# Optimization experiments

Measured on AMD Instinct MI355X. Metric: run time of the kernel, lower is better.

The kernel has to match this reference:

```python
import jax, jax.numpy as jnp
import numpy as np

N, E, IN_DIM, EMBED_DIM, HID_DIM = 10000, 320000, 128, 128, 64
NEG_SLOPE = 0.2


def setup_inputs() -> dict:
    key = jax.random.key(0)
    ks = jax.random.split(key, 7)
    x = jax.random.normal(ks[0], (N, IN_DIM), dtype=jnp.float32)
    edge_index = jax.random.randint(ks[1], (2, E), 0, N, dtype=jnp.int64)
    dense_w = jax.random.normal(ks[2], (IN_DIM, EMBED_DIM), dtype=jnp.float32) / np.sqrt(IN_DIM)
    dense_b = jnp.zeros((EMBED_DIM,), dtype=jnp.float32)
    gat_w = jax.random.normal(ks[3], (EMBED_DIM, HID_DIM), dtype=jnp.float32) / np.sqrt(EMBED_DIM)
    att_src = jax.random.normal(ks[4], (HID_DIM,), dtype=jnp.float32) * 0.1
    att_dst = jax.random.normal(ks[5], (HID_DIM,), dtype=jnp.float32) * 0.1
    gat_b = jnp.zeros((HID_DIM,), dtype=jnp.float32)
    return {"x": x, "edge_index": edge_index, "dense_w": dense_w, "dense_b": dense_b,
            "gat_w": gat_w, "att_src": att_src, "att_dst": att_dst, "gat_b": gat_b}


def reference(x, edge_index, dense_w, dense_b, gat_w, att_src, att_dst, gat_b):
    n = x.shape[0]
    # dense + relu
    h = jax.nn.relu(x @ dense_w + dense_b)            # [N, embed]
    # GATConv (heads=1): linear transform
    z = h @ gat_w                                     # [N, hid]
    # add self loops (PyG default)
    loops = jnp.arange(n, dtype=edge_index.dtype)
    src = jnp.concatenate([edge_index[0], loops])     # [E+N] message source j
    dst = jnp.concatenate([edge_index[1], loops])     # [E+N] message target i
    a_src = z @ att_src                               # [N]
    a_dst = z @ att_dst                               # [N]
    e = jax.nn.leaky_relu(a_src[src] + a_dst[dst], NEG_SLOPE)  # [E+N]
    # segment softmax over incoming edges of each target node
    m = jax.ops.segment_max(e, dst, num_segments=n)
    ex = jnp.exp(e - m[dst])
    denom = jax.ops.segment_sum(ex, dst, num_segments=n)
    alpha = ex / denom[dst]                           # [E+N]
    embed_x = jax.ops.segment_sum(alpha[:, None] * z[src], dst, num_segments=n) + gat_b  # [N, hid]
    # pairwise sigmoid similarity
    sim = jax.nn.sigmoid(embed_x @ embed_x.T)         # [N, N]
    return sim, embed_x
```

## Files before the change

### kernel.cpp

```cpp
#include <hip/hip_runtime.h>
#include <math.h>

#define N_NODES 10000
#define E_EDGES 320000
#define IN_DIM 128
#define EMB 128
#define HID 64
#define NEG_SLOPE 0.2f

typedef __attribute__((ext_vector_type(8))) short short8;
typedef __attribute__((ext_vector_type(4))) short short4_t;
typedef __attribute__((ext_vector_type(4))) float floatx4;
typedef __attribute__((ext_vector_type(4))) int   intx4;
typedef __attribute__((ext_vector_type(2))) int   intx2;

__device__ __forceinline__ short f2bf(float f) {
    unsigned u = __float_as_uint(f);
    unsigned r = u + 0x7fffu + ((u >> 16) & 1u);
    return (short)(r >> 16);
}

__device__ __forceinline__ float sigmoidf_fast(float v) {
    return __builtin_amdgcn_rcpf(1.f + __expf(-v));
}

__global__ __launch_bounds__(256) void dense_gat_kernel(
    const float* __restrict__ x, const float* __restrict__ dw,
    const float* __restrict__ db, const float* __restrict__ gw,
    const float* __restrict__ asv, const float* __restrict__ adv,
    float* __restrict__ z, float* __restrict__ a_src, float* __restrict__ a_dst)
{
    __shared__ float xs[16][IN_DIM];
    __shared__ float hs[16][EMB];
    __shared__ float wsm[32 * 128];
    const int t = threadIdx.x;
    const int row0 = blockIdx.x * 16;

    #pragma unroll
    for (int r = 0; r < 2; ++r) {
        const int idx = t + r * 256;
        const int row = idx >> 5, c4 = idx & 31;
        *(floatx4*)&xs[row][c4 * 4] =
            *(const floatx4*)&x[(row0 + row) * IN_DIM + c4 * 4];
    }

    const int col = t & 127, rb = (t >> 7) * 8;
    float acc[8];
    {
        const float bias = db[col];
        #pragma unroll
        for (int r = 0; r < 8; ++r) acc[r] = bias;
    }
    for (int ch = 0; ch < 4; ++ch) {
        __syncthreads();
        #pragma unroll
        for (int r = 0; r < 4; ++r) {
            const int idx = t + r * 256;
            const int row = idx >> 5, c4 = idx & 31;
            *(floatx4*)&wsm[row * 128 + c4 * 4] =
                *(const floatx4*)&dw[(ch * 32 + row) * EMB + c4 * 4];
        }
        __syncthreads();
        #pragma unroll
        for (int jg = 0; jg < 8; ++jg) {
            const int jb = jg * 4;
            floatx4 xr[8];
            #pragma unroll
            for (int r = 0; r < 8; ++r)
                xr[r] = *(const floatx4*)&xs[rb + r][ch * 32 + jb];
            float wv[4];
            #pragma unroll
            for (int k = 0; k < 4; ++k) wv[k] = wsm[(jb + k) * 128 + col];
            #pragma unroll
            for (int k = 0; k < 4; ++k)
                #pragma unroll
                for (int r = 0; r < 8; ++r) acc[r] = fmaf(xr[r][k], wv[k], acc[r]);
        }
    }
    #pragma unroll
    for (int r = 0; r < 8; ++r) hs[rb + r][col] = fmaxf(acc[r], 0.f);

    const int col2 = t & 63, rb2 = (t >> 6) * 4;
    float acc2[4] = {0.f, 0.f, 0.f, 0.f};
    for (int ch = 0; ch < 2; ++ch) {
        __syncthreads();
        #pragma unroll
        for (int r = 0; r < 4; ++r) {
            const int idx = t + r * 256;
            const int row = idx >> 4, c4 = idx & 15;
            *(floatx4*)&wsm[row * 64 + c4 * 4] =
                *(const floatx4*)&gw[(ch * 64 + row) * HID + c4 * 4];
        }
        __syncthreads();
        #pragma unroll
        for (int kg = 0; kg < 16; ++kg) {
            const int kb = kg * 4;
            floatx4 hr[4];
            #pragma unroll
            for (int r = 0; r < 4; ++r)
                hr[r] = *(const floatx4*)&hs[rb2 + r][ch * 64 + kb];
            float gv[4];
            #pragma unroll
            for (int k = 0; k < 4; ++k) gv[k] = wsm[(kb + k) * 64 + col2];
            #pragma unroll
            for (int k = 0; k < 4; ++k)
                #pragma unroll
                for (int r = 0; r < 4; ++r) acc2[r] = fmaf(hr[r][k], gv[k], acc2[r]);
        }
    }

    const float as_c = asv[col2], ad_c = adv[col2];
    #pragma unroll
    for (int r = 0; r < 4; ++r) {
        z[(row0 + rb2 + r) * HID + col2] = acc2[r];
        float ps = acc2[r] * as_c;
        float pd = acc2[r] * ad_c;
        #pragma unroll
        for (int off = 32; off > 0; off >>= 1) {
            ps += __shfl_down(ps, off, 64);
            pd += __shfl_down(pd, off, 64);
        }
        if ((t & 63) == 0) {
            a_src[row0 + rb2 + r] = ps;
            a_dst[row0 + rb2 + r] = pd;
        }
    }
}

__global__ __launch_bounds__(256) void count_kernel(
    const int* __restrict__ ei, int* __restrict__ cnt)
{
    const int e = blockIdx.x * blockDim.x + threadIdx.x;
    const int total = E_EDGES + N_NODES;
    if (e >= total) return;
    int s, d;
    if (e < E_EDGES) { s = ei[e]; d = ei[E_EDGES + e]; }
    else             { s = d = e - E_EDGES; }
    if ((unsigned)s >= N_NODES || (unsigned)d >= N_NODES) return;
    atomicAdd(&cnt[d], 1);
}

__global__ __launch_bounds__(256) void scan_kernel(
    const int* __restrict__ cnt, int* __restrict__ offs, int* __restrict__ cursor)
{
    __shared__ int scnt[10240];
    __shared__ int part[256];
    const int t = threadIdx.x;
    #pragma unroll
    for (int r = 0; r < 10; ++r) {
        const int i4 = t + r * 256;
        intx4 v = {0, 0, 0, 0};
        if (i4 < 2500) v = *(const intx4*)&cnt[i4 * 4];
        *(intx4*)&scnt[i4 * 4] = v;
    }
    __syncthreads();
    const int base = t * 40;
    int vals[40];
    int local = 0;
    #pragma unroll
    for (int i = 0; i < 40; ++i) { vals[i] = scnt[base + i]; local += vals[i]; }
    part[t] = local;
    __syncthreads();
    for (int off = 1; off < 256; off <<= 1) {
        const int v = (t >= off) ? part[t - off] : 0;
        __syncthreads();
        part[t] += v;
        __syncthreads();
    }
    int running = (t == 0) ? 0 : part[t - 1];
    #pragma unroll
    for (int i = 0; i < 40; ++i) {
        const int idx = base + i;
        if (idx < N_NODES) { offs[idx] = running; cursor[idx] = running; }
        running += vals[i];
    }
    if (t == 255) offs[N_NODES] = running;
}

__global__ __launch_bounds__(256) void scatter_kernel(
    const int* __restrict__ ei, const float* __restrict__ a_src,
    const float* __restrict__ a_dst, int* __restrict__ cursor,
    intx2* __restrict__ se)
{
    const int e = blockIdx.x * blockDim.x + threadIdx.x;
    const int total = E_EDGES + N_NODES;
    if (e >= total) return;
    int s, d;
    if (e < E_EDGES) { s = ei[e]; d = ei[E_EDGES + e]; }
    else             { s = d = e - E_EDGES; }
    if ((unsigned)s >= N_NODES || (unsigned)d >= N_NODES) return;
    float v = a_src[s] + a_dst[d];
    v = (v > 0.f) ? v : NEG_SLOPE * v;
    const float w = __expf(v);
    const int pos = atomicAdd(&cursor[d], 1);
    intx2 p;
    p[0] = s;
    p[1] = __float_as_int(w);
    se[pos] = p;
}

__global__ __launch_bounds__(256) void aggregate_kernel(
    const int* __restrict__ offs, const intx2* __restrict__ se,
    const float* __restrict__ z, const float* __restrict__ gb,
    float* __restrict__ emb)
{
    const int wid  = (blockIdx.x * blockDim.x + threadIdx.x) >> 6;
    const int lane = threadIdx.x & 63;
    if (wid >= N_NODES) return;
    const int beg = offs[wid], end = offs[wid + 1];
    float acc = 0.f, sw = 0.f;
    int i = beg;
    for (; i + 2 <= end; i += 2) {
        const intx2 p0 = se[i];
        const intx2 p1 = se[i + 1];
        const float z0 = z[p0[0] * HID + lane];
        const float z1 = z[p1[0] * HID + lane];
        const float w0 = __int_as_float(p0[1]);
        const float w1 = __int_as_float(p1[1]);
        acc = fmaf(w0, z0, acc);
        acc = fmaf(w1, z1, acc);
        sw += w0 + w1;
    }
    if (i < end) {
        const intx2 p = se[i];
        const float w = __int_as_float(p[1]);
        acc = fmaf(w, z[p[0] * HID + lane], acc);
        sw += w;
    }
    emb[wid * HID + lane] = acc / sw + gb[lane];
}

#define SROW 72
__global__ __launch_bounds__(256) void sim_kernel(
    const float* __restrict__ emb, float* __restrict__ sim)
{
    __shared__ short As[128 * SROW];
    __shared__ short Bs[128 * SROW];
    const int t    = threadIdx.x;
    const int lane = t & 63;
    const int wave = t >> 6;
    const int wm   = (wave >> 1) * 64;
    const int wn   = (wave & 1) * 64;
    const int l15  = lane & 15;
    const int quad = lane >> 4;

    int bi, bj;
    {
        const int gx = blockIdx.x, gy = blockIdx.y;
        if (gy <= gx) { bi = gy; bj = gx; }
        else          { bi = 40 + gx; bj = 79 + gx - gy; }
    }

    #pragma unroll
    for (int round = 0; round < 8; ++round) {
        const int idx = t + round * 256;
        const int row = idx >> 4, c4 = idx & 15;
        int gr = bi * 128 + row; if (gr > N_NODES - 1) gr = N_NODES - 1;
        int gc = bj * 128 + row; if (gc > N_NODES - 1) gc = N_NODES - 1;
        const floatx4 a = *(const floatx4*)&emb[gr * HID + c4 * 4];
        const floatx4 b = *(const floatx4*)&emb[gc * HID + c4 * 4];
        short4_t sa, sb;
        #pragma unroll
        for (int j = 0; j < 4; ++j) { sa[j] = f2bf(a[j]); sb[j] = f2bf(b[j]); }
        *(short4_t*)&As[row * SROW + c4 * 4] = sa;
        *(short4_t*)&Bs[row * SROW + c4 * 4] = sb;
    }
    __syncthreads();

    short8 afrag[4][2];
    #pragma unroll
    for (int ti = 0; ti < 4; ++ti)
        #pragma unroll
        for (int ks = 0; ks < 2; ++ks)
            afrag[ti][ks] = *(const short8*)&As[(wm + ti * 16 + l15) * SROW +
                                                ks * 32 + quad * 8];

    floatx4 acc[4][4];
    const floatx4 zero = {0.f, 0.f, 0.f, 0.f};
    #pragma unroll
    for (int ti = 0; ti < 4; ++ti)
        #pragma unroll
        for (int tj = 0; tj < 4; ++tj) acc[ti][tj] = zero;

    #pragma unroll
    for (int tj = 0; tj < 4; ++tj) {
        const short8 bf0 = *(const short8*)&Bs[(wn + tj * 16 + l15) * SROW + quad * 8];
        const short8 bf1 = *(const short8*)&Bs[(wn + tj * 16 + l15) * SROW + 32 + quad * 8];
        #pragma unroll
        for (int ti = 0; ti < 4; ++ti) {
            acc[ti][tj] = __builtin_amdgcn_mfma_f32_16x16x32_bf16(
                afrag[ti][0], bf0, acc[ti][tj], 0, 0, 0);
            acc[ti][tj] = __builtin_amdgcn_mfma_f32_16x16x32_bf16(
                afrag[ti][1], bf1, acc[ti][tj], 0, 0, 0);
        }
    }
    __syncthreads();

    float* const scr0 = (float*)As;
    float* const scr1 = (float*)Bs;
    const int srow0 = (wave >> 1) * 16 + quad * 4;

    #pragma unroll
    for (int ti = 0; ti < 4; ++ti) {
        float* const scr = (ti & 1) ? scr1 : scr0;
        #pragma unroll
        for (int reg = 0; reg < 4; ++reg)
            #pragma unroll
            for (int tj = 0; tj < 4; ++tj)
                scr[(srow0 + reg) * 132 + wn + tj * 16 + l15] =
                    sigmoidf_fast(acc[ti][tj][reg]);
        __syncthreads();

        #pragma unroll
        for (int round = 0; round < 4; ++round) {
            const int idx = t + round * 256;
            const int rr = idx >> 5, c4 = idx & 31;
            const floatx4 v4 = *(const floatx4*)&scr[rr * 132 + c4 * 4];
            const int grow = bi * 128 +
                ((rr < 16) ? (ti * 16 + rr) : (64 + ti * 16 + rr - 16));
            const int gcol = bj * 128 + c4 * 4;
            if (grow < N_NODES && gcol < N_NODES)
                *(floatx4*)&sim[(unsigned)grow * N_NODES + gcol] = v4;
        }
        if (bi != bj) {
            #pragma unroll
            for (int round = 0; round < 4; ++round) {
                const int idx = t + round * 256;
                const int kq  = idx & 3;
                const int gcl = (idx >> 2) & 127;
                const int blk = idx >> 9;
                floatx4 v4;
                #pragma unroll
                for (int m = 0; m < 4; ++m)
                    v4[m] = scr[(blk * 16 + kq * 4 + m) * 132 + gcl];
                const int trow = bj * 128 + gcl;
                const int tcol = bi * 128 + blk * 64 + ti * 16 + kq * 4;
                if (trow < N_NODES && tcol < N_NODES)
                    *(floatx4*)&sim[(unsigned)trow * N_NODES + tcol] = v4;
            }
        }
    }
}

extern "C" void kernel_launch(void* const* d_in, const int* in_sizes, int n_in,
                              void* d_out, int out_size, void* d_ws, size_t ws_size,
                              hipStream_t stream)
{
    const float* x   = (const float*)d_in[0];
    const int*   ei  = (const int*)d_in[1];
    const float* dw  = (const float*)d_in[2];
    const float* db  = (const float*)d_in[3];
    const float* gw  = (const float*)d_in[4];
    const float* asv = (const float*)d_in[5];
    const float* adv = (const float*)d_in[6];
    const float* gb  = (const float*)d_in[7];

    float* out = (float*)d_out;
    float* sim = out;
    float* emb = out + (size_t)N_NODES * N_NODES;

    const size_t need = 1350002u * sizeof(float);
    float* ws = (ws_size >= need) ? (float*)d_ws : out;
    float* z      = ws;
    float* a_src  = ws + 640000;
    float* a_dst  = ws + 650000;
    int*   cnt    = (int*)(ws + 660000);
    int*   offs   = (int*)(ws + 670000);
    int*   cursor = (int*)(ws + 680001);
    intx2* se     = (intx2*)(ws + 690002);

    hipMemsetAsync(cnt, 0, N_NODES * sizeof(int), stream);

    dense_gat_kernel<<<N_NODES / 16, 256, 0, stream>>>(x, dw, db, gw, asv, adv,
                                                       z, a_src, a_dst);

    const int total_edges = E_EDGES + N_NODES;
    const int eb = (total_edges + 255) / 256;
    count_kernel<<<eb, 256, 0, stream>>>(ei, cnt);
    scan_kernel<<<1, 256, 0, stream>>>(cnt, offs, cursor);
    scatter_kernel<<<eb, 256, 0, stream>>>(ei, a_src, a_dst, cursor, se);
    aggregate_kernel<<<(N_NODES * 64 + 255) / 256, 256, 0, stream>>>(
        offs, se, z, gb, emb);

    dim3 grid(79, 40);
    sim_kernel<<<grid, 256, 0, stream>>>(emb, sim);
}
```

Baseline: 614.7 us.

## Vectorize GAT aggregation across edges and stage full sim tile in LDS

The aggregation kernel now splits each wave into four lane groups. Each group handles every fourth edge and loads z as float4, and the partial sums are combined with cross-lane shuffles. The similarity kernel's epilogue writes the whole 128x128 sigmoid tile into one padded LDS buffer (stride 133) behind a single barrier, instead of four passes of 32 rows with a barrier each. It then streams out the direct tile and the transposed tile. This cuts barriers and makes the transposed reads simpler, but it raises LDS use to about 68KB per block, which can lower occupancy, and the float4 LDS reads at an odd row stride are unaligned.

Measured after the change: 563.9 us. 8.3% less time.

```diff
diff --git a/kernel.cpp b/kernel.cpp
--- a/kernel.cpp
+++ b/kernel.cpp
@@ -207,35 +207,41 @@
     const int wid  = (blockIdx.x * blockDim.x + threadIdx.x) >> 6;
     const int lane = threadIdx.x & 63;
     if (wid >= N_NODES) return;
+    const int g  = lane >> 4;
+    const int c4 = (lane & 15) * 4;
     const int beg = offs[wid], end = offs[wid + 1];
-    float acc = 0.f, sw = 0.f;
-    int i = beg;
-    for (; i + 2 <= end; i += 2) {
-        const intx2 p0 = se[i];
-        const intx2 p1 = se[i + 1];
-        const float z0 = z[p0[0] * HID + lane];
-        const float z1 = z[p1[0] * HID + lane];
-        const float w0 = __int_as_float(p0[1]);
-        const float w1 = __int_as_float(p1[1]);
-        acc = fmaf(w0, z0, acc);
-        acc = fmaf(w1, z1, acc);
-        sw += w0 + w1;
-    }
-    if (i < end) {
+    floatx4 acc = {0.f, 0.f, 0.f, 0.f};
+    float sw = 0.f;
+    for (int i = beg + g; i < end; i += 4) {
         const intx2 p = se[i];
+        const floatx4 zv = *(const floatx4*)&z[p[0] * HID + c4];
         const float w = __int_as_float(p[1]);
-        acc = fmaf(w, z[p[0] * HID + lane], acc);
-        sw += w;
-    }
-    emb[wid * HID + lane] = acc / sw + gb[lane];
+        acc += zv * w;
+        sw  += w;
+    }
+    #pragma unroll
+    for (int off = 16; off <= 32; off <<= 1) {
+        #pragma unroll
+        for (int k = 0; k < 4; ++k) acc[k] += __shfl_xor(acc[k], off, 64);
+        sw += __shfl_xor(sw, off, 64);
+    }
+    if (g == 0) {
+        const floatx4 gv = *(const floatx4*)&gb[c4];
+        floatx4 r;
+        #pragma unroll
+        for (int k = 0; k < 4; ++k) r[k] = acc[k] / sw + gv[k];
+        *(floatx4*)&emb[wid * HID + c4] = r;
+    }
 }
 
 #define SROW 72
+#define SCR_STRIDE 133
 __global__ __launch_bounds__(256) void sim_kernel(
     const float* __restrict__ emb, float* __restrict__ sim)
 {
-    __shared__ short As[128 * SROW];
-    __shared__ short Bs[128 * SROW];
+    __shared__ float smem[128 * SCR_STRIDE];
+    short* const As = (short*)smem;
+    short* const Bs = (short*)smem + 128 * SROW;
     const int t    = threadIdx.x;
     const int lane = t & 63;
     const int wave = t >> 6;
@@ -296,47 +302,40 @@
     }
     __syncthreads();
 
-    float* const scr0 = (float*)As;
-    float* const scr1 = (float*)Bs;
-    const int srow0 = (wave >> 1) * 16 + quad * 4;
-
-    #pragma unroll
-    for (int ti = 0; ti < 4; ++ti) {
-        float* const scr = (ti & 1) ? scr1 : scr0;
+    #pragma unroll
+    for (int ti = 0; ti < 4; ++ti)
         #pragma unroll
         for (int reg = 0; reg < 4; ++reg)
             #pragma unroll
             for (int tj = 0; tj < 4; ++tj)
-                scr[(srow0 + reg) * 132 + wn + tj * 16 + l15] =
-                    sigmoidf_fast(acc[ti][tj][reg]);
-        __syncthreads();
-
-        #pragma unroll
-        for (int round = 0; round < 4; ++round) {
+                smem[(wm + ti * 16 + quad * 4 + reg) * SCR_STRIDE +
+                     wn + tj * 16 + l15] = sigmoidf_fast(acc[ti][tj][reg]);
+    __syncthreads();
+
+    #pragma unroll
+    for (int round = 0; round < 16; ++round) {
+        const int idx = t + round * 256;
+        const int rr = idx >> 5, cq = idx & 31;
+        const int grow = bi * 128 + rr;
+        const int gcol = bj * 128 + cq * 4;
+        if (grow < N_NODES && gcol < N_NODES) {
+            const floatx4 v4 = *(const floatx4*)&smem[rr * SCR_STRIDE + cq * 4];
+            *(floatx4*)&sim[(unsigned)grow * N_NODES + gcol] = v4;
+        }
+    }
+    if (bi != bj) {
+        #pragma unroll
+        for (int round = 0; round < 16; ++round) {
             const int idx = t + round * 256;
-            const int rr = idx >> 5, c4 = idx & 31;
-            const floatx4 v4 = *(const floatx4*)&scr[rr * 132 + c4 * 4];
-            const int grow = bi * 128 +
-                ((rr < 16) ? (ti * 16 + rr) : (64 + ti * 16 + rr - 16));
-            const int gcol = bj * 128 + c4 * 4;
-            if (grow < N_NODES && gcol < N_NODES)
-                *(floatx4*)&sim[(unsigned)grow * N_NODES + gcol] = v4;
-        }
-        if (bi != bj) {
-            #pragma unroll
-            for (int round = 0; round < 4; ++round) {
-                const int idx = t + round * 256;
-                const int kq  = idx & 3;
-                const int gcl = (idx >> 2) & 127;
-                const int blk = idx >> 9;
+            const int rr = idx >> 5, cq = idx & 31;
+            const int trow = bj * 128 + rr;
+            const int tcol = bi * 128 + cq * 4;
+            if (trow < N_NODES && tcol < N_NODES) {
                 floatx4 v4;
                 #pragma unroll
                 for (int m = 0; m < 4; ++m)
-                    v4[m] = scr[(blk * 16 + kq * 4 + m) * 132 + gcl];
-                const int trow = bj * 128 + gcl;
-                const int tcol = bi * 128 + blk * 64 + ti * 16 + kq * 4;
-                if (trow < N_NODES && tcol < N_NODES)
-                    *(floatx4*)&sim[(unsigned)trow * N_NODES + tcol] = v4;
+                    v4[m] = smem[(cq * 4 + m) * SCR_STRIDE + rr];
+                *(floatx4*)&sim[(unsigned)trow * N_NODES + tcol] = v4;
             }
         }
     }
```
